# Optimization experiments

Hardware: AMD Instinct MI355X
Metric: run time of the kernel (lower is better)

Reference implementation:

```python
import jax, jax.numpy as jnp
import numpy as np

K = 512
HIDDEN = 256


def setup_inputs() -> dict:
    key = jax.random.key(0)
    k1, k2 = jax.random.split(key)
    z = jax.random.normal(k1, (8, 8192, HIDDEN), dtype=jnp.float32)
    # codebook init: uniform(-1/k, 1/k) as in the torch module
    codebook = jax.random.uniform(k2, (K, HIDDEN), dtype=jnp.float32,
                                  minval=-1.0 / K, maxval=1.0 / K)
    return {"z": z, "codebook": codebook}


def reference(z, codebook):
    # squared L2 distance to every code, expanded form to avoid the
    # [N, k, hidden] intermediate: ||z||^2 - 2 z.c + ||c||^2
    z2 = jnp.sum(z * z, axis=-1, keepdims=True)            # [B, T, 1]
    c2 = jnp.sum(codebook * codebook, axis=-1)             # [k]
    cross = jnp.einsum('bth,kh->btk', z, codebook)         # [B, T, k]
    distances = z2 - 2.0 * cross + c2                      # [B, T, k]
    ind = jnp.argmin(distances, axis=-1)                   # [B, T] int
    z_q = codebook[ind]                                    # [B, T, hidden]

    vq_loss = jnp.mean((z_q - jax.lax.stop_gradient(z)) ** 2)
    commitment_loss = jnp.mean((z - jax.lax.stop_gradient(z_q)) ** 2)
    z_q_st = z + jax.lax.stop_gradient(z_q - z)
    return (z_q_st, ind, vq_loss + commitment_loss)
```

## Files before the change

kernel.cpp:

```cpp
#include <hip/hip_runtime.h>

#define M_TOKENS 65536
#define HID      256
#define KCODES   512

#define IND_OFF  (M_TOKENS * HID)
#define LOSS_OFF (IND_OFF + M_TOKENS)

#define TAU      1.5e-4f

#define WS_C2_OFF        16
#define WS_BHI_OFF       4096
#define WS_BLO_OFF       (4096 + 262144)
#define WS_LIST_OFF_FAST (4096 + 524288)
#define WS_LIST_OFF_SLOW 4096
#define WS_MIN_FAST      (WS_LIST_OFF_FAST + 8192 * 4)

typedef __attribute__((ext_vector_type(8))) short  short8;
typedef __attribute__((ext_vector_type(4))) float  f32x4;

__device__ inline unsigned short f2bf(float f) {
    unsigned u = __float_as_uint(f);
    u += 0x7FFF + ((u >> 16) & 1);
    return (unsigned short)(u >> 16);
}
__device__ inline float bf2f(unsigned short h) {
    return __uint_as_float(((unsigned)h) << 16);
}

__global__ __launch_bounds__(256) void vq_prep(
    const float* __restrict__ cb,
    unsigned short* __restrict__ Bhi, unsigned short* __restrict__ Blo,
    float* __restrict__ c2, double* __restrict__ acc, int* __restrict__ cnt) {
    int b = blockIdx.x;
    if (b < 64) {
        int g = b * 256 + threadIdx.x;
        int frag = g >> 6, lane = g & 63;
        int nb = frag >> 3, kb = frag & 7;
        int code = nb * 16 + (lane & 15);
        int kk = kb * 32 + (lane >> 4) * 8;
        const float4* s4 = reinterpret_cast<const float4*>(cb + code * HID + kk);
        float4 v0 = s4[0], v1 = s4[1];
        float f[8] = {v0.x, v0.y, v0.z, v0.w, v1.x, v1.y, v1.z, v1.w};
        short8 vh, vl;
        #pragma unroll
        for (int j = 0; j < 8; ++j) {
            unsigned short h = f2bf(f[j]);
            vh[j] = (short)h;
            vl[j] = (short)f2bf(f[j] - bf2f(h));
        }
        *reinterpret_cast<short8*>(Bhi + (size_t)g * 8) = vh;
        *reinterpret_cast<short8*>(Blo + (size_t)g * 8) = vl;
    } else {
        if (b == 64 && threadIdx.x == 0) { *acc = 0.0; *cnt = 0; }
        int k = (b - 64) * 256 + threadIdx.x;
        const float* row = cb + k * HID;
        double s = 0.0;
        for (int i = 0; i < HID; ++i) {
            double v = (double)row[i];
            s = fma(v, v, s);
        }
        c2[k] = (float)s;
    }
}

__global__ __launch_bounds__(256, 2) void vq_main_mfma(
    const float* __restrict__ z, const float* __restrict__ cb,
    const float* __restrict__ c2g,
    const unsigned short* __restrict__ Bhi,
    const unsigned short* __restrict__ Blo,
    float* __restrict__ out, double* __restrict__ loss_acc,
    int* __restrict__ cnt, int* __restrict__ list, int cap) {

    __shared__ short8 ldsB[3][16][64];
    __shared__ float  lds_c2[KCODES];

    const int tid  = threadIdx.x;
    const int wid  = tid >> 6;
    const int lane = tid & 63;
    const int q    = lane >> 4;
    const int tokW = blockIdx.x * 128 + wid * 32;

    const float4* z4  = reinterpret_cast<const float4*>(z);
    const float4* cb4 = reinterpret_cast<const float4*>(cb);

    lds_c2[tid]       = c2g[tid];
    lds_c2[tid + 256] = c2g[tid + 256];

#define STAGE(nbv, bufv) do {                                                  \
        _Pragma("unroll")                                                      \
        for (int j = 0; j < 4; ++j) {                                          \
            int f_  = (wid << 2) | j;                                          \
            int kb_ = f_ & 7;                                                  \
            const unsigned short* src_ =                                       \
                ((f_ < 8) ? Bhi : Blo) +                                       \
                (((size_t)((nbv) * 8 + kb_) * 64 + lane) << 3);                \
            __builtin_amdgcn_global_load_lds(                                  \
                (const __attribute__((address_space(1))) void*)src_,           \
                (__attribute__((address_space(3))) void*)&ldsB[bufv][f_][0],   \
                16, 0, 0);                                                     \
        }                                                                      \
    } while (0)

    short8 ah[2][8], al[2][8];
    float sq[2];
    #pragma unroll
    for (int mf = 0; mf < 2; ++mf) {
        int token = tokW + mf * 16 + (lane & 15);
        const float4* zr = z4 + (size_t)token * 64 + q * 2;
        float s = 0.f;
        #pragma unroll
        for (int kb = 0; kb < 8; ++kb) {
            float4 v0 = zr[kb * 8];
            float4 v1 = zr[kb * 8 + 1];
            float f[8] = {v0.x, v0.y, v0.z, v0.w, v1.x, v1.y, v1.z, v1.w};
            short8 vh, vl;
            #pragma unroll
            for (int j = 0; j < 8; ++j) {
                unsigned short h = f2bf(f[j]);
                vh[j] = (short)h;
                vl[j] = (short)f2bf(f[j] - bf2f(h));
                s = fmaf(f[j], f[j], s);
            }
            ah[mf][kb] = vh;
            al[mf][kb] = vl;
        }
        s += __shfl_xor(s, 16, 64);
        s += __shfl_xor(s, 32, 64);
        sq[mf] = s;
    }

    STAGE(0, 0);
    STAGE(1, 1);
    asm volatile("s_waitcnt lgkmcnt(0)" ::: "memory");

    float b1[2][4], b2[2][4];
    int   i1[2][4];
    #pragma unroll
    for (int mf = 0; mf < 2; ++mf)
        #pragma unroll
        for (int r = 0; r < 4; ++r) { b1[mf][r] = 3.4e38f; b2[mf][r] = 3.4e38f; i1[mf][r] = 0; }

    int bcur = 0, bnx2 = 2;
    for (int nb = 0; nb < 32; ++nb) {
        asm volatile("s_waitcnt vmcnt(4)" ::: "memory");
        __builtin_amdgcn_s_barrier();
        __builtin_amdgcn_sched_barrier(0);

        STAGE((nb + 2) & 31, bnx2);

        f32x4 a0 = {0.f, 0.f, 0.f, 0.f};
        f32x4 a1 = {0.f, 0.f, 0.f, 0.f};
        #pragma unroll
        for (int kb = 0; kb < 8; ++kb) {
            short8 vbh = ldsB[bcur][kb][lane];
            short8 vbl = ldsB[bcur][8 + kb][lane];
            a0 = __builtin_amdgcn_mfma_f32_16x16x32_bf16(ah[0][kb], vbh, a0, 0, 0, 0);
            a1 = __builtin_amdgcn_mfma_f32_16x16x32_bf16(ah[1][kb], vbh, a1, 0, 0, 0);
            a0 = __builtin_amdgcn_mfma_f32_16x16x32_bf16(al[0][kb], vbh, a0, 0, 0, 0);
            a1 = __builtin_amdgcn_mfma_f32_16x16x32_bf16(al[1][kb], vbh, a1, 0, 0, 0);
            a0 = __builtin_amdgcn_mfma_f32_16x16x32_bf16(ah[0][kb], vbl, a0, 0, 0, 0);
            a1 = __builtin_amdgcn_mfma_f32_16x16x32_bf16(ah[1][kb], vbl, a1, 0, 0, 0);
        }
        int code = nb * 16 + (lane & 15);
        float c2v = lds_c2[code];
        #pragma unroll
        for (int r = 0; r < 4; ++r) {
            float s0 = fmaf(-2.f, a0[r], c2v);
            if (s0 < b1[0][r]) { b2[0][r] = b1[0][r]; b1[0][r] = s0; i1[0][r] = code; }
            else if (s0 < b2[0][r]) b2[0][r] = s0;
            float s1 = fmaf(-2.f, a1[r], c2v);
            if (s1 < b1[1][r]) { b2[1][r] = b1[1][r]; b1[1][r] = s1; i1[1][r] = code; }
            else if (s1 < b2[1][r]) b2[1][r] = s1;
        }
        bcur = (bcur == 2) ? 0 : bcur + 1;
        bnx2 = (bnx2 == 2) ? 0 : bnx2 + 1;
    }
#undef STAGE

    #pragma unroll
    for (int st = 1; st <= 8; st <<= 1) {
        #pragma unroll
        for (int mf = 0; mf < 2; ++mf)
            #pragma unroll
            for (int r = 0; r < 4; ++r) {
                float ob1 = __shfl_xor(b1[mf][r], st, 64);
                int   oi1 = __shfl_xor(i1[mf][r], st, 64);
                float ob2 = __shfl_xor(b2[mf][r], st, 64);
                if (ob1 < b1[mf][r] || (ob1 == b1[mf][r] && oi1 < i1[mf][r])) {
                    b2[mf][r] = fminf(b1[mf][r], ob2);
                    b1[mf][r] = ob1;
                    i1[mf][r] = oi1;
                } else {
                    b2[mf][r] = fminf(b2[mf][r], ob1);
                }
            }
    }

    if ((lane & 15) == 0) {
        #pragma unroll
        for (int mf = 0; mf < 2; ++mf) {
            float4 iv;
            #pragma unroll
            for (int r = 0; r < 4; ++r) {
                ((float*)&iv)[r] = (float)i1[mf][r];
                if (b2[mf][r] - b1[mf][r] <= TAU) {
                    int pos = atomicAdd(cnt, 1);
                    if (pos < cap) list[pos] = tokW + mf * 16 + q * 4 + r;
                }
            }
            *reinterpret_cast<float4*>(out + IND_OFF + tokW + mf * 16 + q * 4) = iv;
        }
    }

    double lsum = 0.0;
    #pragma unroll
    for (int mf = 0; mf < 2; ++mf)
        #pragma unroll
        for (int r = 0; r < 4; ++r) {
            float z2r = __shfl(sq[mf], (lane & 48) | (q * 4 + r), 64);
            if ((lane & 15) == 0) lsum += (double)z2r + (double)b1[mf][r];
        }
    lsum += __shfl_xor(lsum, 16, 64);
    lsum += __shfl_xor(lsum, 32, 64);
    if (lane == 0) atomicAdd(loss_acc, lsum);

    float4* out4 = reinterpret_cast<float4*>(out);
    #pragma unroll
    for (int tt = 0; tt < 32; ++tt) {
        int code = __shfl(i1[tt >> 4][tt & 3], ((tt >> 2) & 3) * 16, 64);
        float4 cv = cb4[(size_t)code * 64 + lane];
        out4[(size_t)(tokW + tt) * 64 + lane] = cv;
    }
}

#define BM   128
#define NC   128
#define KS   32
#define PAD  33

__global__ void vq_init(const float* __restrict__ cb, float* __restrict__ c2,
                        double* __restrict__ acc, int* __restrict__ cnt) {
    int k = threadIdx.x;
    if (k == 0) { *acc = 0.0; *cnt = 0; }
    const float* row = cb + k * HID;
    double s = 0.0;
    for (int i = 0; i < HID; ++i) {
        double v = (double)row[i];
        s = fma(v, v, s);
    }
    c2[k] = (float)s;
}

__global__ __launch_bounds__(256, 2) void vq_main_f32(
    const float* __restrict__ z, const float* __restrict__ cb,
    const float* __restrict__ c2g, float* __restrict__ out,
    double* __restrict__ loss_acc, int* __restrict__ cnt,
    int* __restrict__ list, int cap) {

    __shared__ float smem[(BM + NC) * PAD];
    float* zs = smem;
    float* cs = smem + BM * PAD;

    const int tid = threadIdx.x;
    const int tx = tid & 15;
    const int ty = tid >> 4;
    const int tokBase = blockIdx.x * BM;

    const float4* z4g  = reinterpret_cast<const float4*>(z);
    const float4* cb4g = reinterpret_cast<const float4*>(cb);

    float bs[8], bs2[8];
    int   bi[8];
    #pragma unroll
    for (int m = 0; m < 8; ++m) { bs[m] = 3.4e38f; bs2[m] = 3.4e38f; bi[m] = 0; }

    for (int chunk = 0; chunk < KCODES / NC; ++chunk) {
        float acc[8][8];
        #pragma unroll
        for (int m = 0; m < 8; ++m)
            #pragma unroll
            for (int n = 0; n < 8; ++n) acc[m][n] = 0.f;

        for (int ks = 0; ks < HID / KS; ++ks) {
            __syncthreads();
            #pragma unroll
            for (int i = 0; i < 4; ++i) {
                int f   = tid + i * 256;
                int row = f >> 3;
                int k4  = f & 7;
                float4 zv = z4g[(tokBase + row) * (HID / 4) + ks * (KS / 4) + k4];
                int b = row * PAD + k4 * 4;
                zs[b + 0] = zv.x; zs[b + 1] = zv.y; zs[b + 2] = zv.z; zs[b + 3] = zv.w;
                float4 cv = cb4g[(chunk * NC + row) * (HID / 4) + ks * (KS / 4) + k4];
                cs[b + 0] = cv.x; cs[b + 1] = cv.y; cs[b + 2] = cv.z; cs[b + 3] = cv.w;
            }
            __syncthreads();

            #pragma unroll 2
            for (int k = 0; k < KS; ++k) {
                float zf[8], cf[8];
                #pragma unroll
                for (int m = 0; m < 8; ++m) zf[m] = zs[(ty * 8 + m) * PAD + k];
                #pragma unroll
                for (int n = 0; n < 8; ++n) cf[n] = cs[(tx * 8 + n) * PAD + k];
                #pragma unroll
                for (int m = 0; m < 8; ++m)
                    #pragma unroll
                    for (int n = 0; n < 8; ++n)
                        acc[m][n] = fmaf(zf[m], cf[n], acc[m][n]);
            }
        }

        #pragma unroll
        for (int n = 0; n < 8; ++n) {
            int code = chunk * NC + tx * 8 + n;
            float c2v = c2g[code];
            #pragma unroll
            for (int m = 0; m < 8; ++m) {
                float s = fmaf(-2.f, acc[m][n], c2v);
                if (s < bs[m]) { bs2[m] = bs[m]; bs[m] = s; bi[m] = code; }
                else if (s < bs2[m]) bs2[m] = s;
            }
        }
    }

    __syncthreads();
    float* rs   = smem;
    int*   ri   = reinterpret_cast<int*>(smem + BM * 16);
    float* rs2  = smem + BM * 32;
    int*   inds = reinterpret_cast<int*>(smem + BM * 48);
    float* wred = smem + BM * 48 + BM;

    #pragma unroll
    for (int m = 0; m < 8; ++m) {
        int tok = ty * 8 + m;
        rs [tok * 16 + tx] = bs[m];
        ri [tok * 16 + tx] = bi[m];
        rs2[tok * 16 + tx] = bs2[m];
    }
    __syncthreads();

    if (tid < BM) {
        float B1 = rs[tid * 16];
        int   I1 = ri[tid * 16];
        float B2 = rs2[tid * 16];
        for (int j = 1; j < 16; ++j) {
            float b1v = rs [tid * 16 + j];
            int   i1v = ri [tid * 16 + j];
            float b2v = rs2[tid * 16 + j];
            if (b1v < B1 || (b1v == B1 && i1v < I1)) {
                B2 = fminf(B1, b2v); B1 = b1v; I1 = i1v;
            } else {
                B2 = fminf(B2, b1v);
            }
        }
        inds[tid] = I1;
        out[IND_OFF + tokBase + tid] = (float)I1;
        if (B2 - B1 <= TAU) {
            int pos = atomicAdd(cnt, 1);
            if (pos < cap) list[pos] = tokBase + tid;
        }
    }
    __syncthreads();

    float loc = 0.f;
    float4* out4 = reinterpret_cast<float4*>(out);
    for (int it = 0; it < (BM * HID / 4) / 256; ++it) {
        int e4  = it * 256 + tid;
        int tok = e4 >> 6;
        int h4  = e4 & 63;
        int code = inds[tok];
        float4 cv = cb4g[code * 64 + h4];
        float4 zv = z4g[(tokBase + tok) * 64 + h4];
        out4[(tokBase + tok) * 64 + h4] = cv;
        float dx = cv.x - zv.x, dy = cv.y - zv.y;
        float dz = cv.z - zv.z, dw = cv.w - zv.w;
        loc = fmaf(dx, dx, loc);
        loc = fmaf(dy, dy, loc);
        loc = fmaf(dz, dz, loc);
        loc = fmaf(dw, dw, loc);
    }
    #pragma unroll
    for (int off = 32; off > 0; off >>= 1) loc += __shfl_xor(loc, off, 64);
    int wave = tid >> 6;
    if ((tid & 63) == 0) wred[wave] = loc;
    __syncthreads();
    if (tid == 0) {
        double t = (double)wred[0] + (double)wred[1] +
                   (double)wred[2] + (double)wred[3];
        atomicAdd(loss_acc, t);
    }
}

__global__ __launch_bounds__(256) void vq_refine(
    const float* __restrict__ z, const float* __restrict__ cb,
    const float* __restrict__ c2g, const double* __restrict__ loss_acc,
    const int* __restrict__ cnt, const int* __restrict__ list,
    float* __restrict__ out, int cap) {

    if (blockIdx.x == 0 && threadIdx.x == 0)
        out[LOSS_OFF] = (float)(2.0 * (*loss_acc) / (double)(M_TOKENS * HID));

    __shared__ float  zrow[HID];
    __shared__ double red_d[256];
    __shared__ int    red_i[256];

    const int tid = threadIdx.x;
    int n = *cnt; if (n > cap) n = cap;

    for (int idx = blockIdx.x; idx < n; idx += gridDim.x) {
        int t = list[idx];
        float zi = z[t * HID + tid];
        zrow[tid] = zi;
        red_d[tid] = (double)zi * (double)zi;
        __syncthreads();
        for (int s = 128; s > 0; s >>= 1) {
            if (tid < s) red_d[tid] += red_d[tid + s];
            __syncthreads();
        }
        float z2f = (float)red_d[0];
        __syncthreads();

        const float4* zr4 = reinterpret_cast<const float4*>(zrow);
        const float4* c0  = reinterpret_cast<const float4*>(cb + tid * HID);
        const float4* c1  = reinterpret_cast<const float4*>(cb + (tid + 256) * HID);
        double p00 = 0, p01 = 0, p02 = 0, p03 = 0;
        double p10 = 0, p11 = 0, p12 = 0, p13 = 0;
        #pragma unroll 4
        for (int i = 0; i < HID / 4; ++i) {
            float4 zv = zr4[i];
            float4 a = c0[i];
            float4 b = c1[i];
            p00 = fma((double)zv.x, (double)a.x, p00);
            p01 = fma((double)zv.y, (double)a.y, p01);
            p02 = fma((double)zv.z, (double)a.z, p02);
            p03 = fma((double)zv.w, (double)a.w, p03);
            p10 = fma((double)zv.x, (double)b.x, p10);
            p11 = fma((double)zv.y, (double)b.y, p11);
            p12 = fma((double)zv.z, (double)b.z, p12);
            p13 = fma((double)zv.w, (double)b.w, p13);
        }
        double bestD = 1e300; int bestK = 1 << 30;
        #pragma unroll
        for (int c = 0; c < 2; ++c) {
            int k = tid + c * 256;
            double accd = (c == 0) ? ((p00 + p01) + (p02 + p03))
                                   : ((p10 + p11) + (p12 + p13));
            float cross32 = (float)accd;
            float u = 2.0f * cross32;
            float tq = (float)((double)z2f - (double)u);
            double v = (double)tq + (double)c2g[k];
            float D = (float)v;
            double Dd = (double)D;
            if (Dd < bestD || (Dd == bestD && k < bestK)) { bestD = Dd; bestK = k; }
        }
        red_d[tid] = bestD; red_i[tid] = bestK;
        __syncthreads();
        for (int s = 128; s > 0; s >>= 1) {
            if (tid < s) {
                double d2 = red_d[tid + s]; int i2 = red_i[tid + s];
                if (d2 < red_d[tid] || (d2 == red_d[tid] && i2 < red_i[tid])) {
                    red_d[tid] = d2; red_i[tid] = i2;
                }
            }
            __syncthreads();
        }
        int best = red_i[0];
        if (tid == 0) out[IND_OFF + t] = (float)best;
        out[t * HID + tid] = cb[best * HID + tid];
        __syncthreads();
    }
}

extern "C" void kernel_launch(void* const* d_in, const int* in_sizes, int n_in,
                              void* d_out, int out_size, void* d_ws, size_t ws_size,
                              hipStream_t stream) {
    const float* z  = (const float*)d_in[0];
    const float* cb = (const float*)d_in[1];
    float* out = (float*)d_out;
    double* acc = (double*)d_ws;
    int*  cnt = (int*)((char*)d_ws + 8);
    float* c2 = (float*)((char*)d_ws + WS_C2_OFF);

    if (ws_size >= WS_MIN_FAST) {
        unsigned short* Bhi = (unsigned short*)((char*)d_ws + WS_BHI_OFF);
        unsigned short* Blo = (unsigned short*)((char*)d_ws + WS_BLO_OFF);
        int* list = (int*)((char*)d_ws + WS_LIST_OFF_FAST);
        int cap = 8192;
        vq_prep<<<66, 256, 0, stream>>>(cb, Bhi, Blo, c2, acc, cnt);
        vq_main_mfma<<<M_TOKENS / 128, 256, 0, stream>>>(
            z, cb, c2, Bhi, Blo, out, acc, cnt, list, cap);
        vq_refine<<<512, 256, 0, stream>>>(z, cb, c2, acc, cnt, list, out, cap);
    } else {
        int* list = (int*)((char*)d_ws + WS_LIST_OFF_SLOW);
        int cap = 0;
        if (ws_size > WS_LIST_OFF_SLOW + 16) {
            size_t avail = (ws_size - WS_LIST_OFF_SLOW) / 4;
            cap = (avail > 8192) ? 8192 : (int)avail;
        }
        vq_init<<<1, 512, 0, stream>>>(cb, c2, acc, cnt);
        vq_main_f32<<<M_TOKENS / BM, 256, 0, stream>>>(
            z, cb, c2, out, acc, cnt, list, cap);
        vq_refine<<<512, 256, 0, stream>>>(z, cb, c2, acc, cnt, list, out, cap);
    }
}
```

Baseline: 181.0 us.

## Restructure codebook staging into double-buffered 32-code chunks with MFMA priority

```diff
diff --git a/kernel.cpp b/kernel.cpp
--- a/kernel.cpp
+++ b/kernel.cpp
@@ -72,7 +72,7 @@
     float* __restrict__ out, double* __restrict__ loss_acc,
     int* __restrict__ cnt, int* __restrict__ list, int cap) {
 
-    __shared__ short8 ldsB[3][16][64];
+    __shared__ short8 ldsB[2][32][64];
     __shared__ float  lds_c2[KCODES];
 
     const int tid  = threadIdx.x;
@@ -87,20 +87,24 @@
     lds_c2[tid]       = c2g[tid];
     lds_c2[tid + 256] = c2g[tid + 256];
 
-#define STAGE(nbv, bufv) do {                                                  \
+#define STAGE(kv, bufv) do {                                                   \
         _Pragma("unroll")                                                      \
-        for (int j = 0; j < 4; ++j) {                                          \
-            int f_  = (wid << 2) | j;                                          \
-            int kb_ = f_ & 7;                                                  \
+        for (int j = 0; j < 8; ++j) {                                          \
+            int s_  = (wid << 3) | j;                                          \
+            int g_  = s_ >> 4;                                                 \
+            int t_  = s_ & 15;                                                 \
+            int kb_ = t_ & 7;                                                  \
             const unsigned short* src_ =                                       \
-                ((f_ < 8) ? Bhi : Blo) +                                       \
-                (((size_t)((nbv) * 8 + kb_) * 64 + lane) << 3);                \
+                ((t_ < 8) ? Bhi : Blo) +                                       \
+                (((size_t)((2 * (kv) + g_) * 8 + kb_) * 64 + lane) << 3);      \
             __builtin_amdgcn_global_load_lds(                                  \
                 (const __attribute__((address_space(1))) void*)src_,           \
-                (__attribute__((address_space(3))) void*)&ldsB[bufv][f_][0],   \
+                (__attribute__((address_space(3))) void*)&ldsB[bufv][s_][0],   \
                 16, 0, 0);                                                     \
         }                                                                      \
     } while (0)
+
+    STAGE(0, 0);
 
     short8 ah[2][8], al[2][8];
     float sq[2];
@@ -130,10 +134,6 @@
         sq[mf] = s;
     }
 
-    STAGE(0, 0);
-    STAGE(1, 1);
-    asm volatile("s_waitcnt lgkmcnt(0)" ::: "memory");
-
     float b1[2][4], b2[2][4];
     int   i1[2][4];
     #pragma unroll
@@ -141,40 +141,41 @@
         #pragma unroll
         for (int r = 0; r < 4; ++r) { b1[mf][r] = 3.4e38f; b2[mf][r] = 3.4e38f; i1[mf][r] = 0; }
 
-    int bcur = 0, bnx2 = 2;
-    for (int nb = 0; nb < 32; ++nb) {
-        asm volatile("s_waitcnt vmcnt(4)" ::: "memory");
-        __builtin_amdgcn_s_barrier();
-        __builtin_amdgcn_sched_barrier(0);
-
-        STAGE((nb + 2) & 31, bnx2);
-
-        f32x4 a0 = {0.f, 0.f, 0.f, 0.f};
-        f32x4 a1 = {0.f, 0.f, 0.f, 0.f};
-        #pragma unroll
-        for (int kb = 0; kb < 8; ++kb) {
-            short8 vbh = ldsB[bcur][kb][lane];
-            short8 vbl = ldsB[bcur][8 + kb][lane];
-            a0 = __builtin_amdgcn_mfma_f32_16x16x32_bf16(ah[0][kb], vbh, a0, 0, 0, 0);
-            a1 = __builtin_amdgcn_mfma_f32_16x16x32_bf16(ah[1][kb], vbh, a1, 0, 0, 0);
-            a0 = __builtin_amdgcn_mfma_f32_16x16x32_bf16(al[0][kb], vbh, a0, 0, 0, 0);
-            a1 = __builtin_amdgcn_mfma_f32_16x16x32_bf16(al[1][kb], vbh, a1, 0, 0, 0);
-            a0 = __builtin_amdgcn_mfma_f32_16x16x32_bf16(ah[0][kb], vbl, a0, 0, 0, 0);
-            a1 = __builtin_amdgcn_mfma_f32_16x16x32_bf16(ah[1][kb], vbl, a1, 0, 0, 0);
-        }
-        int code = nb * 16 + (lane & 15);
-        float c2v = lds_c2[code];
-        #pragma unroll
-        for (int r = 0; r < 4; ++r) {
-            float s0 = fmaf(-2.f, a0[r], c2v);
-            if (s0 < b1[0][r]) { b2[0][r] = b1[0][r]; b1[0][r] = s0; i1[0][r] = code; }
-            else if (s0 < b2[0][r]) b2[0][r] = s0;
-            float s1 = fmaf(-2.f, a1[r], c2v);
-            if (s1 < b1[1][r]) { b2[1][r] = b1[1][r]; b1[1][r] = s1; i1[1][r] = code; }
-            else if (s1 < b2[1][r]) b2[1][r] = s1;
-        }
-        bcur = (bcur == 2) ? 0 : bcur + 1;
-        bnx2 = (bnx2 == 2) ? 0 : bnx2 + 1;
+    #pragma unroll 2
+    for (int k = 0; k < 16; ++k) {
+        int buf = k & 1;
+        __syncthreads();
+        if (k < 15) STAGE(k + 1, buf ^ 1);
+
+        #pragma unroll
+        for (int g = 0; g < 2; ++g) {
+            f32x4 a0 = {0.f, 0.f, 0.f, 0.f};
+            f32x4 a1 = {0.f, 0.f, 0.f, 0.f};
+            __builtin_amdgcn_s_setprio(1);
+            #pragma unroll
+            for (int kb = 0; kb < 8; ++kb) {
+                short8 vbh = ldsB[buf][g * 16 + kb][lane];
+                short8 vbl = ldsB[buf][g * 16 + 8 + kb][lane];
+                a0 = __builtin_amdgcn_mfma_f32_16x16x32_bf16(ah[0][kb], vbh, a0, 0, 0, 0);
+                a1 = __builtin_amdgcn_mfma_f32_16x16x32_bf16(ah[1][kb], vbh, a1, 0, 0, 0);
+                a0 = __builtin_amdgcn_mfma_f32_16x16x32_bf16(al[0][kb], vbh, a0, 0, 0, 0);
+                a1 = __builtin_amdgcn_mfma_f32_16x16x32_bf16(al[1][kb], vbh, a1, 0, 0, 0);
+                a0 = __builtin_amdgcn_mfma_f32_16x16x32_bf16(ah[0][kb], vbl, a0, 0, 0, 0);
+                a1 = __builtin_amdgcn_mfma_f32_16x16x32_bf16(ah[1][kb], vbl, a1, 0, 0, 0);
+            }
+            __builtin_amdgcn_s_setprio(0);
+            int code = (2 * k + g) * 16 + (lane & 15);
+            float c2v = lds_c2[code];
+            #pragma unroll
+            for (int r = 0; r < 4; ++r) {
+                float s0 = fmaf(-2.f, a0[r], c2v);
+                if (s0 < b1[0][r]) { b2[0][r] = b1[0][r]; b1[0][r] = s0; i1[0][r] = code; }
+                else if (s0 < b2[0][r]) b2[0][r] = s0;
+                float s1 = fmaf(-2.f, a1[r], c2v);
+                if (s1 < b1[1][r]) { b2[1][r] = b1[1][r]; b1[1][r] = s1; i1[1][r] = code; }
+                else if (s1 < b2[1][r]) b2[1][r] = s1;
+            }
+        }
     }
 #undef STAGE
 
@@ -491,7 +492,7 @@
         vq_prep<<<66, 256, 0, stream>>>(cb, Bhi, Blo, c2, acc, cnt);
         vq_main_mfma<<<M_TOKENS / 128, 256, 0, stream>>>(
             z, cb, c2, Bhi, Blo, out, acc, cnt, list, cap);
-        vq_refine<<<512, 256, 0, stream>>>(z, cb, c2, acc, cnt, list, out, cap);
+        vq_refine<<<256, 256, 0, stream>>>(z, cb, c2, acc, cnt, list, out, cap);
     } else {
         int* list = (int*)((char*)d_ws + WS_LIST_OFF_SLOW);
         int cap = 0;
@@ -502,6 +503,6 @@
         vq_init<<<1, 512, 0, stream>>>(cb, c2, acc, cnt);
         vq_main_f32<<<M_TOKENS / BM, 256, 0, stream>>>(
             z, cb, c2, out, acc, cnt, list, cap);
-        vq_refine<<<512, 256, 0, stream>>>(z, cb, c2, acc, cnt, list, out, cap);
-    }
-}
+        vq_refine<<<256, 256, 0, stream>>>(z, cb, c2, acc, cnt, list, out, cap);
+    }
+}
```

Result: faster. 176.4 us (-2.5%).
